# Kernel optimization log

Measured on AMD Instinct MI355X. Metric: run time of the kernel, lower is better.

## Reference

```python
import jax, jax.numpy as jnp
import numpy as np

BLOCK_M, BLOCK_K = 16, 64
THRES = 0.8


def setup_inputs() -> dict:
    key = jax.random.key(0)
    kx, kw = jax.random.split(key)
    bsz, seq, in_f, out_f = 128, 1, 4096, 11008
    x = jax.random.normal(kx, (bsz, seq, in_f), dtype=jnp.float16)
    # kaiming_uniform_(a=sqrt(5)) on a (in,out) weight -> bound = 1/sqrt(fan_in)
    bound = 1.0 / np.sqrt(in_f)
    weight = jax.random.uniform(kw, (in_f, out_f), dtype=jnp.float16,
                                minval=-bound, maxval=bound)
    bias = jnp.zeros((out_f,), dtype=jnp.float16)
    return {"x": x, "weight": weight, "bias": bias}


def reference(x, weight, bias):
    bsz, seq, hidden = x.shape
    x2 = x.reshape(bsz * seq, hidden)          # (M, K), seq == 1 decode path
    M, K = x2.shape
    # avg_magnitude_threshold: per (BLOCK_M, BLOCK_K) block mean |x| vs thres
    blocks = x2.reshape(M // BLOCK_M, BLOCK_M, K // BLOCK_K, BLOCK_K)
    avg = jnp.mean(jnp.abs(blocks).astype(jnp.float32), axis=(1, 3))  # (M/bm, K/bk)
    mask = avg > THRES                           # block active if avg magnitude above thres
    # blocksparse_masked_gemm: skipped blocks contribute nothing -> zero them out
    xm = jnp.where(mask[:, None, :, None], blocks, jnp.float16(0)).reshape(M, K)
    y = xm @ weight                              # (M, out_features)
    return y.reshape(bsz, seq, -1) + bias
```

## Files before the change

### kernel.cpp

```cpp
#include <hip/hip_runtime.h>
#include <stdint.h>

using f32x4   = __attribute__((ext_vector_type(4))) float;
using short8  = __attribute__((ext_vector_type(8))) short;
using float4v = __attribute__((ext_vector_type(4))) float;
using float2v = __attribute__((ext_vector_type(2))) float;
using uint2v  = __attribute__((ext_vector_type(2))) unsigned int;
using uint4v  = __attribute__((ext_vector_type(4))) unsigned int;

#define NCOL 11008
#define KDIM 4096
#define BSTRIDE 72

__device__ __forceinline__ unsigned pk_bf16(float a, float b) {
  unsigned ua = __float_as_uint(a); ua += 0x7fffu + ((ua >> 16) & 1u);
  unsigned ub = __float_as_uint(b); ub += 0x7fffu + ((ub >> 16) & 1u);
  return (ua >> 16) | (ub & 0xffff0000u);
}

__global__ __launch_bounds__(256) void mask_convert_kernel(
    const float* __restrict__ x, unsigned* __restrict__ xbf) {
  const int rb = blockIdx.x;
  const int g  = blockIdx.y;
  const int t  = threadIdx.x;
  __shared__ double part[256];
  __shared__ unsigned sh_bits;

  const float* base = x + (size_t)rb * 16 * KDIM + g * 512 + t * 2;
  double s = 0.0;
#pragma unroll
  for (int r = 0; r < 16; ++r) {
    float2v a = *(const float2v*)(base + (size_t)r * KDIM);
    s += (double)fabsf(a[0]) + (double)fabsf(a[1]);
  }
  part[t] = s;
  __syncthreads();
  if (t < 8) {
    double acc = 0.0;
#pragma unroll
    for (int u = 0; u < 32; ++u) acc += part[t * 32 + u];
    bool on = (acc * (1.0 / 1024.0)) > (double)0.8f;
    unsigned long long bal = __ballot(on);
    if (t == 0) sh_bits = (unsigned)(bal & 0xffu);
  }
  __syncthreads();
  const unsigned keep = (sh_bits >> (t >> 5)) & 1u;

  unsigned* dst = xbf + (size_t)rb * 16 * (KDIM / 2) + g * 256 + t;
#pragma unroll
  for (int r = 0; r < 16; ++r) {
    float2v a = *(const float2v*)(base + (size_t)r * KDIM);
    dst[(size_t)r * (KDIM / 2)] = keep ? pk_bf16(a[0], a[1]) : 0u;
  }
}

__global__ __launch_bounds__(256) void gemm_kernel(
    const unsigned* __restrict__ xbf, const float* __restrict__ w,
    const float* __restrict__ bias, float* __restrict__ out) {

  __shared__ __align__(16) uint8_t lds[2 * 64 * BSTRIDE];

  const int tid  = threadIdx.x;
  const int lane = tid & 63;
  const int wv   = tid >> 6;
  const int c    = lane & 15;
  const int q    = lane >> 4;
  const int n0   = blockIdx.x * 32;

  f32x4 acc[2][2] = {};

  const int sk = tid >> 3;
  const int sn = (tid & 7) * 4;
  const size_t wOff = (size_t)sk * NCOL + n0 + sn;

  float4v wr0, wr1;
#define ISSUE_W(KB)                                                       \
  {                                                                       \
    const float* wp = w + (size_t)(KB) * 64 * NCOL + wOff;                \
    wr0 = *(const float4v*)(wp);                                          \
    wr1 = *(const float4v*)(wp + (size_t)32 * NCOL);                      \
  }

  const uint4v* aB0 = (const uint4v*)xbf + (size_t)((wv * 2 + 0) * 16 + c) * (KDIM / 8) + q;
  const uint4v* aB1 = (const uint4v*)xbf + (size_t)((wv * 2 + 1) * 16 + c) * (KDIM / 8) + q;

  ISSUE_W(0);
  int p = 0;
  for (int kb = 0; kb < 64; ++kb) {
    uint8_t* buf = lds + p * 64 * BSTRIDE;
    {
      uint2v v;
      v[0] = pk_bf16(wr0[0], wr0[1]);
      v[1] = pk_bf16(wr0[2], wr0[3]);
      *(uint2v*)(buf + (size_t)sk * BSTRIDE + sn * 2) = v;
      uint2v u;
      u[0] = pk_bf16(wr1[0], wr1[1]);
      u[1] = pk_bf16(wr1[2], wr1[3]);
      *(uint2v*)(buf + (size_t)(sk + 32) * BSTRIDE + sn * 2) = u;
    }
    if (kb < 63) ISSUE_W(kb + 1);
    __syncthreads();

#pragma unroll
    for (int ks = 0; ks < 2; ++ks) {
      union { uint4v u; short8 v; } a0, a1;
      a0.u = aB0[kb * 8 + ks * 4];
      a1.u = aB1[kb * 8 + ks * 4];

      const uint8_t* wb = buf + (size_t)(ks * 32 + q * 8) * BSTRIDE + c * 4;
      unsigned wj[8];
#pragma unroll
      for (int j = 0; j < 8; ++j)
        wj[j] = *(const unsigned*)(wb + (size_t)j * BSTRIDE);
      union { short8 v; unsigned u[4]; } be, bo;
#pragma unroll
      for (int pp = 0; pp < 4; ++pp) {
        be.u[pp] = (wj[2 * pp] & 0x0000ffffu) | (wj[2 * pp + 1] << 16);
        bo.u[pp] = (wj[2 * pp] >> 16) | (wj[2 * pp + 1] & 0xffff0000u);
      }
      acc[0][0] = __builtin_amdgcn_mfma_f32_16x16x32_bf16(a0.v, be.v, acc[0][0], 0, 0, 0);
      acc[0][1] = __builtin_amdgcn_mfma_f32_16x16x32_bf16(a0.v, bo.v, acc[0][1], 0, 0, 0);
      acc[1][0] = __builtin_amdgcn_mfma_f32_16x16x32_bf16(a1.v, be.v, acc[1][0], 0, 0, 0);
      acc[1][1] = __builtin_amdgcn_mfma_f32_16x16x32_bf16(a1.v, bo.v, acc[1][1], 0, 0, 0);
    }
    p ^= 1;
  }
#undef ISSUE_W

  const int colE = n0 + 2 * c;
  const float bE = bias[colE];
  const float bO = bias[colE + 1];
#pragma unroll
  for (int b = 0; b < 2; ++b) {
#pragma unroll
    for (int pp = 0; pp < 4; ++pp) {
      const int row = (wv * 2 + b) * 16 + q * 4 + pp;
      float2v st;
      st[0] = acc[b][0][pp] + bE;
      st[1] = acc[b][1][pp] + bO;
      *(float2v*)(out + (size_t)row * NCOL + colE) = st;
    }
  }
}

extern "C" void kernel_launch(void* const* d_in, const int* in_sizes, int n_in,
                              void* d_out, int out_size, void* d_ws, size_t ws_size,
                              hipStream_t stream) {
  const float* x    = (const float*)d_in[0];
  const float* w    = (const float*)d_in[1];
  const float* bias = (const float*)d_in[2];
  float* out        = (float*)d_out;
  unsigned* xbf     = (unsigned*)d_ws;

  hipLaunchKernelGGL(mask_convert_kernel, dim3(8, 8), dim3(256), 0, stream, x, xbf);
  hipLaunchKernelGGL(gemm_kernel, dim3(344), dim3(256), 0, stream,
                     xbf, w, bias, out);
}
```

Before: 288.0 us.

## Split GEMM over K segments with atomic accumulation and direct global-to-LDS loads

The GEMM grid is split four ways along K, so 1376 blocks run instead of 344, and partial sums are combined with relaxed float atomics into an output pre-filled with bias by a new kernel. Weight tiles are copied straight from global memory into LDS as fp32 with global_load_lds, and the bf16 conversion moves to the point where the tiles are read from LDS. The aim is better occupancy and memory-level parallelism for a weight-streaming, bandwidth-bound GEMM. The cost is an extra launch, atomic traffic on the output, doubled LDS per block, and summation order that varies from run to run.

```diff
diff --git a/kernel.cpp b/kernel.cpp
--- a/kernel.cpp
+++ b/kernel.cpp
@@ -3,14 +3,17 @@
 
 using f32x4   = __attribute__((ext_vector_type(4))) float;
 using short8  = __attribute__((ext_vector_type(8))) short;
-using float4v = __attribute__((ext_vector_type(4))) float;
 using float2v = __attribute__((ext_vector_type(2))) float;
-using uint2v  = __attribute__((ext_vector_type(2))) unsigned int;
 using uint4v  = __attribute__((ext_vector_type(4))) unsigned int;
 
 #define NCOL 11008
 #define KDIM 4096
-#define BSTRIDE 72
+#define KSEG 4
+#define KB_PER_SEG 16
+#define TILE_B 8192
+
+#define AS1 __attribute__((address_space(1)))
+#define AS3 __attribute__((address_space(3)))
 
 __device__ __forceinline__ unsigned pk_bf16(float a, float b) {
   unsigned ua = __float_as_uint(a); ua += 0x7fffu + ((ua >> 16) & 1u);
@@ -54,11 +57,17 @@
   }
 }
 
+__global__ __launch_bounds__(256) void bias_init_kernel(
+    const float* __restrict__ bias, float* __restrict__ out) {
+  const int n = blockIdx.x * 256 + threadIdx.x;
+  out[(size_t)blockIdx.y * NCOL + n] = bias[n];
+}
+
 __global__ __launch_bounds__(256) void gemm_kernel(
     const unsigned* __restrict__ xbf, const float* __restrict__ w,
-    const float* __restrict__ bias, float* __restrict__ out) {
+    float* __restrict__ out) {
 
-  __shared__ __align__(16) uint8_t lds[2 * 64 * BSTRIDE];
+  __shared__ __align__(16) uint8_t lds[2 * TILE_B];
 
   const int tid  = threadIdx.x;
   const int lane = tid & 63;
@@ -66,79 +75,80 @@
   const int c    = lane & 15;
   const int q    = lane >> 4;
   const int n0   = blockIdx.x * 32;
+  const int kb0  = blockIdx.y * KB_PER_SEG;
 
   f32x4 acc[2][2] = {};
 
-  const int sk = tid >> 3;
-  const int sn = (tid & 7) * 4;
-  const size_t wOff = (size_t)sk * NCOL + n0 + sn;
+  const int kA = tid >> 3;
+  const int cB = (tid & 7) * 4;
+  const float* gW = w + (size_t)kA * NCOL + n0 + cB;
 
-  float4v wr0, wr1;
-#define ISSUE_W(KB)                                                       \
-  {                                                                       \
-    const float* wp = w + (size_t)(KB) * 64 * NCOL + wOff;                \
-    wr0 = *(const float4v*)(wp);                                          \
-    wr1 = *(const float4v*)(wp + (size_t)32 * NCOL);                      \
+#define STAGE(PBUF, KBI)                                                     \
+  {                                                                          \
+    const float* g_ = gW + (size_t)(KBI) * 64 * NCOL;                        \
+    __builtin_amdgcn_global_load_lds(                                        \
+        (const AS1 void*)g_,                                                 \
+        (AS3 void*)(lds + (PBUF) * TILE_B + wv * 1024), 16, 0, 0);           \
+    __builtin_amdgcn_global_load_lds(                                        \
+        (const AS1 void*)(g_ + (size_t)32 * NCOL),                           \
+        (AS3 void*)(lds + (PBUF) * TILE_B + 4096 + wv * 1024), 16, 0, 0);    \
   }
 
   const uint4v* aB0 = (const uint4v*)xbf + (size_t)((wv * 2 + 0) * 16 + c) * (KDIM / 8) + q;
   const uint4v* aB1 = (const uint4v*)xbf + (size_t)((wv * 2 + 1) * 16 + c) * (KDIM / 8) + q;
 
-  ISSUE_W(0);
-  int p = 0;
-  for (int kb = 0; kb < 64; ++kb) {
-    uint8_t* buf = lds + p * 64 * BSTRIDE;
-    {
-      uint2v v;
-      v[0] = pk_bf16(wr0[0], wr0[1]);
-      v[1] = pk_bf16(wr0[2], wr0[3]);
-      *(uint2v*)(buf + (size_t)sk * BSTRIDE + sn * 2) = v;
-      uint2v u;
-      u[0] = pk_bf16(wr1[0], wr1[1]);
-      u[1] = pk_bf16(wr1[2], wr1[3]);
-      *(uint2v*)(buf + (size_t)(sk + 32) * BSTRIDE + sn * 2) = u;
-    }
-    if (kb < 63) ISSUE_W(kb + 1);
-    __syncthreads();
+  auto compute = [&](const uint8_t* buf, int kbi) {
+    union { uint4v u; short8 v; } a00, a01, a10, a11;
+    a00.u = aB0[kbi * 8 + 0];
+    a01.u = aB0[kbi * 8 + 4];
+    a10.u = aB1[kbi * 8 + 0];
+    a11.u = aB1[kbi * 8 + 4];
 
 #pragma unroll
     for (int ks = 0; ks < 2; ++ks) {
-      union { uint4v u; short8 v; } a0, a1;
-      a0.u = aB0[kb * 8 + ks * 4];
-      a1.u = aB1[kb * 8 + ks * 4];
-
-      const uint8_t* wb = buf + (size_t)(ks * 32 + q * 8) * BSTRIDE + c * 4;
-      unsigned wj[8];
+      const uint8_t* wb = buf + (size_t)(ks * 32 + q * 8) * 128 + c * 8;
+      float2v r[8];
 #pragma unroll
       for (int j = 0; j < 8; ++j)
-        wj[j] = *(const unsigned*)(wb + (size_t)j * BSTRIDE);
+        r[j] = *(const float2v*)(wb + (size_t)j * 128);
       union { short8 v; unsigned u[4]; } be, bo;
 #pragma unroll
-      for (int pp = 0; pp < 4; ++pp) {
-        be.u[pp] = (wj[2 * pp] & 0x0000ffffu) | (wj[2 * pp + 1] << 16);
-        bo.u[pp] = (wj[2 * pp] >> 16) | (wj[2 * pp + 1] & 0xffff0000u);
+      for (int p = 0; p < 4; ++p) {
+        be.u[p] = pk_bf16(r[2 * p][0], r[2 * p + 1][0]);
+        bo.u[p] = pk_bf16(r[2 * p][1], r[2 * p + 1][1]);
       }
-      acc[0][0] = __builtin_amdgcn_mfma_f32_16x16x32_bf16(a0.v, be.v, acc[0][0], 0, 0, 0);
-      acc[0][1] = __builtin_amdgcn_mfma_f32_16x16x32_bf16(a0.v, bo.v, acc[0][1], 0, 0, 0);
-      acc[1][0] = __builtin_amdgcn_mfma_f32_16x16x32_bf16(a1.v, be.v, acc[1][0], 0, 0, 0);
-      acc[1][1] = __builtin_amdgcn_mfma_f32_16x16x32_bf16(a1.v, bo.v, acc[1][1], 0, 0, 0);
+      const short8 a0 = ks ? a01.v : a00.v;
+      const short8 a1 = ks ? a11.v : a10.v;
+      acc[0][0] = __builtin_amdgcn_mfma_f32_16x16x32_bf16(a0, be.v, acc[0][0], 0, 0, 0);
+      acc[0][1] = __builtin_amdgcn_mfma_f32_16x16x32_bf16(a0, bo.v, acc[0][1], 0, 0, 0);
+      acc[1][0] = __builtin_amdgcn_mfma_f32_16x16x32_bf16(a1, be.v, acc[1][0], 0, 0, 0);
+      acc[1][1] = __builtin_amdgcn_mfma_f32_16x16x32_bf16(a1, bo.v, acc[1][1], 0, 0, 0);
     }
+  };
+
+  STAGE(0, kb0);
+  __syncthreads();
+
+  int p = 0;
+  for (int i = 0; i < KB_PER_SEG; ++i) {
+    if (i + 1 < KB_PER_SEG) STAGE(p ^ 1, kb0 + i + 1);
+    compute(lds + p * TILE_B, kb0 + i);
+    __syncthreads();
     p ^= 1;
   }
-#undef ISSUE_W
+#undef STAGE
 
   const int colE = n0 + 2 * c;
-  const float bE = bias[colE];
-  const float bO = bias[colE + 1];
 #pragma unroll
   for (int b = 0; b < 2; ++b) {
 #pragma unroll
     for (int pp = 0; pp < 4; ++pp) {
       const int row = (wv * 2 + b) * 16 + q * 4 + pp;
-      float2v st;
-      st[0] = acc[b][0][pp] + bE;
-      st[1] = acc[b][1][pp] + bO;
-      *(float2v*)(out + (size_t)row * NCOL + colE) = st;
+      float* pdst = out + (size_t)row * NCOL + colE;
+      __hip_atomic_fetch_add(pdst,     acc[b][0][pp], __ATOMIC_RELAXED,
+                             __HIP_MEMORY_SCOPE_AGENT);
+      __hip_atomic_fetch_add(pdst + 1, acc[b][1][pp], __ATOMIC_RELAXED,
+                             __HIP_MEMORY_SCOPE_AGENT);
     }
   }
 }
@@ -153,6 +163,7 @@
   unsigned* xbf     = (unsigned*)d_ws;
 
   hipLaunchKernelGGL(mask_convert_kernel, dim3(8, 8), dim3(256), 0, stream, x, xbf);
-  hipLaunchKernelGGL(gemm_kernel, dim3(344), dim3(256), 0, stream,
-                     xbf, w, bias, out);
+  hipLaunchKernelGGL(bias_init_kernel, dim3(43, 128), dim3(256), 0, stream, bias, out);
+  hipLaunchKernelGGL(gemm_kernel, dim3(344, KSEG), dim3(256), 0, stream,
+                     xbf, w, out);
 }
```

Result: no change. 288.7 us (+0.2%).
